# Optimization experiments

Hardware: AMD Instinct MI355X
Metric: run time of the kernel (lower is better)

The kernel has to match this reference:

```python
import jax, jax.numpy as jnp
from jax import lax
import numpy as np

B, T, H, NC = 1024, 2048, 64, 10


def setup_inputs() -> dict:
    key = jax.random.key(0)
    ks = jax.random.split(key, 10)
    s_ih = 1.0 / np.sqrt(H)
    inp = {
        "x": jax.random.normal(ks[0], (B, 1, T), dtype=jnp.float32),
        # PyTorch LSTM params: W_ih [4H, input_size=1], W_hh [4H, H], biases [4H]
        "W_ih": jax.random.uniform(ks[1], (4 * H, 1), minval=-s_ih, maxval=s_ih, dtype=jnp.float32),
        "W_hh": jax.random.uniform(ks[2], (4 * H, H), minval=-s_ih, maxval=s_ih, dtype=jnp.float32),
        "b_ih": jax.random.uniform(ks[3], (4 * H,), minval=-s_ih, maxval=s_ih, dtype=jnp.float32),
        "b_hh": jax.random.uniform(ks[4], (4 * H,), minval=-s_ih, maxval=s_ih, dtype=jnp.float32),
        "fc1_w": jax.random.uniform(ks[5], (H, H), minval=-s_ih, maxval=s_ih, dtype=jnp.float32),
        "fc1_b": jax.random.uniform(ks[6], (H,), minval=-s_ih, maxval=s_ih, dtype=jnp.float32),
        "fc2_w": jax.random.uniform(ks[7], (NC, H), minval=-s_ih, maxval=s_ih, dtype=jnp.float32),
        "fc2_b": jax.random.uniform(ks[8], (NC,), minval=-s_ih, maxval=s_ih, dtype=jnp.float32),
    }
    return inp


def _lstm_last_h(x, W_ih, W_hh, b_ih, b_hh):
    # x: [B, 1, T] -> [B, T, 1]
    xs = jnp.swapaxes(x, 1, 2)
    # precompute input projection for all timesteps: [B, T, 4H]
    x_proj = jnp.einsum("bti,gi->btg", xs, W_ih) + b_ih + b_hh
    x_proj = jnp.swapaxes(x_proj, 0, 1)  # [T, B, 4H]
    h0 = jnp.zeros((x.shape[0], H), dtype=x.dtype)
    c0 = jnp.zeros((x.shape[0], H), dtype=x.dtype)

    def step(carry, xp):
        h, c = carry
        g = xp + h @ W_hh.T  # [B, 4H]
        i, f, gg, o = jnp.split(g, 4, axis=-1)  # PyTorch gate order: i, f, g, o
        i = jax.nn.sigmoid(i)
        f = jax.nn.sigmoid(f)
        gg = jnp.tanh(gg)
        o = jax.nn.sigmoid(o)
        c = f * c + i * gg
        h = o * jnp.tanh(c)
        return (h, c), None

    (h_last, _), _ = lax.scan(step, (h0, c0), x_proj)
    return h_last  # [B, H]


def reference(x, W_ih, W_hh, b_ih, b_hh, fc1_w, fc1_b, fc2_w, fc2_b):
    h = _lstm_last_h(x, W_ih, W_hh, b_ih, b_hh)
    h = jax.nn.relu(h @ fc1_w.T + fc1_b)
    return h @ fc2_w.T + fc2_b  # [B, n_classes]
```

## Files before the change

kernel.cpp:

```cpp
#include <hip/hip_runtime.h>
#include <type_traits>


#define T_STEPS 2048
#define HID 64
#define NCLS 10
#define XCH 128
#define ROWS 4

#define KQS 40
#define KTS 168

typedef short bf16x8 __attribute__((ext_vector_type(8)));
typedef float f32x4 __attribute__((ext_vector_type(4)));

__device__ __forceinline__ unsigned short f2bf(float f) {
    unsigned u = __builtin_bit_cast(unsigned, f);
    u = u + 0x7FFFu + ((u >> 16) & 1u);
    return (unsigned short)(u >> 16);
}

__global__ __attribute__((amdgpu_flat_work_group_size(256, 256)))
void lstm_mfma_kernel(
    const float* __restrict__ x,
    const float* __restrict__ W_ih,
    const float* __restrict__ W_hh,
    const float* __restrict__ b_ih,
    const float* __restrict__ b_hh,
    const float* __restrict__ fc1_w,
    const float* __restrict__ fc1_b,
    const float* __restrict__ fc2_w,
    const float* __restrict__ fc2_b,
    float* __restrict__ out)
{
    const int tid  = threadIdx.x;
    const int lane = tid & 63;
    const int w    = tid >> 6;
    const int quad = lane >> 4;
    const int col  = lane & 15;
    const int row0 = blockIdx.x * ROWS;

    const float L2E = 1.4426950408889634f;

    __shared__ __align__(16) char smem[32768];
    short* whi = (short*)smem;
    short (*abuf)[2 * KTS]     = (short(*)[2 * KTS])smem;
    float (*xlds)[XCH + 4]     = (float(*)[XCH + 4])(smem + 1344);
    float (*hf)[HID + 1]       = (float(*)[HID + 1])(smem + 3456);
    float (*r1buf)[HID + 1]    = (float(*)[HID + 1])(smem + 4496);

    for (int idx = tid; idx < 256 * 64; idx += 256) {
        int r_ = idx >> 6;
        int k  = idx & 63;
        int g = r_ >> 6, u = r_ & 63;
        float scg = (g == 2) ? -2.0f * L2E : -L2E;
        float f = W_hh[r_ * 64 + k] * scg;
        int u4 = u >> 4, n = u & 15;
        int kt = k >> 5, kq = (k & 31) >> 3, j = k & 7;
        int off = (((g * 4 + u4) * 2 + kt) * 64 + (kq * 16 + n)) * 8 + j;
        whi[off] = (short)f2bf(f);
    }
    __syncthreads();

    const int u0 = w * 16 + col;
    bf16x8 Bq[4][2];
    f32x4 biasC[4];
    f32x4 zerov = {0.f, 0.f, 0.f, 0.f};
    #pragma unroll
    for (int gg = 0; gg < 4; ++gg) {
        int t_ = gg * 4 + w;
        #pragma unroll
        for (int kt = 0; kt < 2; ++kt) {
            int off = ((t_ * 2 + kt) * 64 + lane) * 8;
            Bq[gg][kt] = *(const bf16x8*)&whi[off];
            asm volatile("" : "+v"(Bq[gg][kt]));
        }
        float scg = (gg == 2) ? -2.0f * L2E : -L2E;
        float bs = (b_ih[gg * HID + u0] + b_hh[gg * HID + u0]) * scg;
        #pragma unroll
        for (int r = 0; r < 4; ++r) biasC[gg][r] = bs;
    }
    __syncthreads();

    for (int idx = tid; idx < 2 * 2 * KTS; idx += 256) ((short*)abuf)[idx] = 0;

    float wih_u[4];
    #pragma unroll
    for (int gg = 0; gg < 4; ++gg) {
        float scg = (gg == 2) ? -2.0f * L2E : -L2E;
        wih_u[gg] = W_ih[gg * HID + u0] * scg;
    }
    float cc = 0.f, hl = 0.f;

    const int ard0 = (lane >> 4) * KQS + ((lane >> 2) & 3) * 8;
    const int awr  = (u0 >> 5) * KTS + ((u0 >> 3) & 3) * KQS + quad * 8 + (u0 & 7);

    const float* xbase = x + (size_t)row0 * T_STEPS;
    __syncthreads();

    auto step = [&](auto cur_c, int tl) __attribute__((always_inline)) {
        constexpr int CUR = decltype(cur_c)::value;
        constexpr int NXT = CUR ^ 1;

        bf16x8 A0 = *(const bf16x8*)&abuf[CUR][ard0];
        bf16x8 A1 = *(const bf16x8*)&abuf[CUR][ard0 + KTS];

        f32x4 alo[4], ahi[4];
        #pragma unroll
        for (int gg = 0; gg < 4; ++gg)
            alo[gg] = __builtin_amdgcn_mfma_f32_16x16x32_bf16(A0, Bq[gg][0], biasC[gg], 0, 0, 0);
        #pragma unroll
        for (int gg = 0; gg < 4; ++gg)
            ahi[gg] = __builtin_amdgcn_mfma_f32_16x16x32_bf16(A1, Bq[gg][1], zerov, 0, 0, 0);

        {
            float xv = xlds[quad][tl];
            float a0 = fmaf(xv, wih_u[0], alo[0][0] + ahi[0][0]);
            float a1 = fmaf(xv, wih_u[1], alo[1][0] + ahi[1][0]);
            float a2 = fmaf(xv, wih_u[2], alo[2][0] + ahi[2][0]);
            float a3 = fmaf(xv, wih_u[3], alo[3][0] + ahi[3][0]);
            float ig = __builtin_amdgcn_rcpf(1.0f + __builtin_amdgcn_exp2f(a0));
            float fg = __builtin_amdgcn_rcpf(1.0f + __builtin_amdgcn_exp2f(a1));
            float gv = fmaf(2.0f, __builtin_amdgcn_rcpf(1.0f + __builtin_amdgcn_exp2f(a2)), -1.0f);
            float og = __builtin_amdgcn_rcpf(1.0f + __builtin_amdgcn_exp2f(a3));
            cc = fmaf(fg, cc, ig * gv);
            float ec = __builtin_amdgcn_exp2f(-2.8853900817779268f * cc);
            float th = fmaf(2.0f, __builtin_amdgcn_rcpf(1.0f + ec), -1.0f);
            hl = og * th;
            unsigned hp;
            asm("v_cvt_pk_bf16_f32 %0, %1, %2" : "=v"(hp) : "v"(hl), "v"(hl));
            abuf[NXT][awr] = (short)hp;
        }
        __syncthreads();
    };

    #pragma unroll 1
    for (int tc = 0; tc < T_STEPS; tc += 2) {
        const int tl = tc & (XCH - 1);
        if (tl == 0) {
            {
                int i = lane;
                const float* src = xbase + (size_t)w * T_STEPS + tc;
                xlds[w][i]      = src[i];
                xlds[w][i + 64] = src[i + 64];
            }
            __syncthreads();
        }
        step(std::integral_constant<int, 0>{}, tl);
        step(std::integral_constant<int, 1>{}, tl + 1);
    }

    hf[quad][u0] = hl;
    __syncthreads();

    if (w < ROWS) {
        float s = fc1_b[lane];
        const float4* wrow = (const float4*)(fc1_w + lane * HID);
        #pragma unroll
        for (int j4 = 0; j4 < HID / 4; ++j4) {
            float4 wv = wrow[j4];
            s = fmaf(hf[w][j4 * 4 + 0], wv.x, s);
            s = fmaf(hf[w][j4 * 4 + 1], wv.y, s);
            s = fmaf(hf[w][j4 * 4 + 2], wv.z, s);
            s = fmaf(hf[w][j4 * 4 + 3], wv.w, s);
        }
        r1buf[w][lane] = fmaxf(s, 0.0f);
    }
    __syncthreads();

    if (tid < ROWS * NCLS) {
        int m = tid / NCLS, cls = tid % NCLS;
        float s = fc2_b[cls];
        const float* w2 = fc2_w + cls * HID;
        #pragma unroll
        for (int j = 0; j < HID; ++j) s = fmaf(r1buf[m][j], w2[j], s);
        out[(size_t)(row0 + m) * NCLS + cls] = s;
    }
}

extern "C" void kernel_launch(void* const* d_in, const int* in_sizes, int n_in,
                              void* d_out, int out_size, void* d_ws, size_t ws_size,
                              hipStream_t stream) {
    const float* x     = (const float*)d_in[0];
    const float* W_ih  = (const float*)d_in[1];
    const float* W_hh  = (const float*)d_in[2];
    const float* b_ih  = (const float*)d_in[3];
    const float* b_hh  = (const float*)d_in[4];
    const float* fc1_w = (const float*)d_in[5];
    const float* fc1_b = (const float*)d_in[6];
    const float* fc2_w = (const float*)d_in[7];
    const float* fc2_b = (const float*)d_in[8];
    float* out = (float*)d_out;

    dim3 grid(256);
    dim3 block(256);
    lstm_mfma_kernel<<<grid, block, 0, stream>>>(x, W_ih, W_hh, b_ih, b_hh,
                                                 fc1_w, fc1_b, fc2_w, fc2_b, out);
}
```

Baseline: 543.8 us.

## Process two independent batch groups per block and halve the grid

Each block now handles eight batch rows as two interleaved 4-row groups with separate hidden-state buffers, sharing the per-step barrier and the register-resident W_hh fragments. The grid drops from 256 to 128 blocks. The aim is to amortize barrier and latency costs across two independent recurrences through instruction-level parallelism. The cost is that half the compute units sit idle and each step does twice the MFMA and transcendental work.

New measurement: 859.4 us. 1.58x slower.

```diff
diff --git a/kernel.cpp b/kernel.cpp
--- a/kernel.cpp
+++ b/kernel.cpp
@@ -6,7 +6,7 @@
 #define HID 64
 #define NCLS 10
 #define XCH 128
-#define ROWS 4
+#define ROWS 8
 
 #define KQS 40
 #define KTS 168
@@ -44,10 +44,11 @@
 
     __shared__ __align__(16) char smem[32768];
     short* whi = (short*)smem;
-    short (*abuf)[2 * KTS]     = (short(*)[2 * KTS])smem;
-    float (*xlds)[XCH + 4]     = (float(*)[XCH + 4])(smem + 1344);
-    float (*hf)[HID + 1]       = (float(*)[HID + 1])(smem + 3456);
-    float (*r1buf)[HID + 1]    = (float(*)[HID + 1])(smem + 4496);
+    short (*abufA)[2 * KTS]    = (short(*)[2 * KTS])smem;
+    short (*abufB)[2 * KTS]    = (short(*)[2 * KTS])(smem + 1344);
+    float (*xlds)[XCH + 4]     = (float(*)[XCH + 4])(smem + 2688);
+    float (*hf)[HID + 1]       = (float(*)[HID + 1])(smem + 6912);
+    float (*r1buf)[HID + 1]    = (float(*)[HID + 1])(smem + 8992);
 
     for (int idx = tid; idx < 256 * 64; idx += 256) {
         int r_ = idx >> 6;
@@ -82,7 +83,7 @@
     }
     __syncthreads();
 
-    for (int idx = tid; idx < 2 * 2 * KTS; idx += 256) ((short*)abuf)[idx] = 0;
+    for (int idx = tid; idx < 2 * 2 * 2 * KTS; idx += 256) ((short*)smem)[idx] = 0;
 
     float wih_u[4];
     #pragma unroll
@@ -90,7 +91,8 @@
         float scg = (gg == 2) ? -2.0f * L2E : -L2E;
         wih_u[gg] = W_ih[gg * HID + u0] * scg;
     }
-    float cc = 0.f, hl = 0.f;
+    float ccA = 0.f, hlA = 0.f;
+    float ccB = 0.f, hlB = 0.f;
 
     const int ard0 = (lane >> 4) * KQS + ((lane >> 2) & 3) * 8;
     const int awr  = (u0 >> 5) * KTS + ((u0 >> 3) & 3) * KQS + quad * 8 + (u0 & 7);
@@ -102,34 +104,60 @@
         constexpr int CUR = decltype(cur_c)::value;
         constexpr int NXT = CUR ^ 1;
 
-        bf16x8 A0 = *(const bf16x8*)&abuf[CUR][ard0];
-        bf16x8 A1 = *(const bf16x8*)&abuf[CUR][ard0 + KTS];
-
-        f32x4 alo[4], ahi[4];
-        #pragma unroll
-        for (int gg = 0; gg < 4; ++gg)
-            alo[gg] = __builtin_amdgcn_mfma_f32_16x16x32_bf16(A0, Bq[gg][0], biasC[gg], 0, 0, 0);
-        #pragma unroll
-        for (int gg = 0; gg < 4; ++gg)
-            ahi[gg] = __builtin_amdgcn_mfma_f32_16x16x32_bf16(A1, Bq[gg][1], zerov, 0, 0, 0);
+        bf16x8 A0a = *(const bf16x8*)&abufA[CUR][ard0];
+        bf16x8 A1a = *(const bf16x8*)&abufA[CUR][ard0 + KTS];
+        bf16x8 A0b = *(const bf16x8*)&abufB[CUR][ard0];
+        bf16x8 A1b = *(const bf16x8*)&abufB[CUR][ard0 + KTS];
+        float xvA = xlds[quad][tl];
+        float xvB = xlds[quad + 4][tl];
+
+        f32x4 aloA[4], ahiA[4], aloB[4], ahiB[4];
+        #pragma unroll
+        for (int gg = 0; gg < 4; ++gg)
+            aloA[gg] = __builtin_amdgcn_mfma_f32_16x16x32_bf16(A0a, Bq[gg][0], biasC[gg], 0, 0, 0);
+        #pragma unroll
+        for (int gg = 0; gg < 4; ++gg)
+            ahiA[gg] = __builtin_amdgcn_mfma_f32_16x16x32_bf16(A1a, Bq[gg][1], zerov, 0, 0, 0);
+        #pragma unroll
+        for (int gg = 0; gg < 4; ++gg)
+            aloB[gg] = __builtin_amdgcn_mfma_f32_16x16x32_bf16(A0b, Bq[gg][0], biasC[gg], 0, 0, 0);
+        #pragma unroll
+        for (int gg = 0; gg < 4; ++gg)
+            ahiB[gg] = __builtin_amdgcn_mfma_f32_16x16x32_bf16(A1b, Bq[gg][1], zerov, 0, 0, 0);
 
         {
-            float xv = xlds[quad][tl];
-            float a0 = fmaf(xv, wih_u[0], alo[0][0] + ahi[0][0]);
-            float a1 = fmaf(xv, wih_u[1], alo[1][0] + ahi[1][0]);
-            float a2 = fmaf(xv, wih_u[2], alo[2][0] + ahi[2][0]);
-            float a3 = fmaf(xv, wih_u[3], alo[3][0] + ahi[3][0]);
+            float a0 = fmaf(xvA, wih_u[0], aloA[0][0] + ahiA[0][0]);
+            float a1 = fmaf(xvA, wih_u[1], aloA[1][0] + ahiA[1][0]);
+            float a2 = fmaf(xvA, wih_u[2], aloA[2][0] + ahiA[2][0]);
+            float a3 = fmaf(xvA, wih_u[3], aloA[3][0] + ahiA[3][0]);
             float ig = __builtin_amdgcn_rcpf(1.0f + __builtin_amdgcn_exp2f(a0));
             float fg = __builtin_amdgcn_rcpf(1.0f + __builtin_amdgcn_exp2f(a1));
             float gv = fmaf(2.0f, __builtin_amdgcn_rcpf(1.0f + __builtin_amdgcn_exp2f(a2)), -1.0f);
             float og = __builtin_amdgcn_rcpf(1.0f + __builtin_amdgcn_exp2f(a3));
-            cc = fmaf(fg, cc, ig * gv);
-            float ec = __builtin_amdgcn_exp2f(-2.8853900817779268f * cc);
+            ccA = fmaf(fg, ccA, ig * gv);
+            float ec = __builtin_amdgcn_exp2f(-2.8853900817779268f * ccA);
             float th = fmaf(2.0f, __builtin_amdgcn_rcpf(1.0f + ec), -1.0f);
-            hl = og * th;
+            hlA = og * th;
             unsigned hp;
-            asm("v_cvt_pk_bf16_f32 %0, %1, %2" : "=v"(hp) : "v"(hl), "v"(hl));
-            abuf[NXT][awr] = (short)hp;
+            asm("v_cvt_pk_bf16_f32 %0, %1, %2" : "=v"(hp) : "v"(hlA), "v"(hlA));
+            abufA[NXT][awr] = (short)hp;
+        }
+        {
+            float a0 = fmaf(xvB, wih_u[0], aloB[0][0] + ahiB[0][0]);
+            float a1 = fmaf(xvB, wih_u[1], aloB[1][0] + ahiB[1][0]);
+            float a2 = fmaf(xvB, wih_u[2], aloB[2][0] + ahiB[2][0]);
+            float a3 = fmaf(xvB, wih_u[3], aloB[3][0] + ahiB[3][0]);
+            float ig = __builtin_amdgcn_rcpf(1.0f + __builtin_amdgcn_exp2f(a0));
+            float fg = __builtin_amdgcn_rcpf(1.0f + __builtin_amdgcn_exp2f(a1));
+            float gv = fmaf(2.0f, __builtin_amdgcn_rcpf(1.0f + __builtin_amdgcn_exp2f(a2)), -1.0f);
+            float og = __builtin_amdgcn_rcpf(1.0f + __builtin_amdgcn_exp2f(a3));
+            ccB = fmaf(fg, ccB, ig * gv);
+            float ec = __builtin_amdgcn_exp2f(-2.8853900817779268f * ccB);
+            float th = fmaf(2.0f, __builtin_amdgcn_rcpf(1.0f + ec), -1.0f);
+            hlB = og * th;
+            unsigned hp;
+            asm("v_cvt_pk_bf16_f32 %0, %1, %2" : "=v"(hp) : "v"(hlB), "v"(hlB));
+            abufB[NXT][awr] = (short)hp;
         }
         __syncthreads();
     };
@@ -140,9 +168,12 @@
         if (tl == 0) {
             {
                 int i = lane;
-                const float* src = xbase + (size_t)w * T_STEPS + tc;
-                xlds[w][i]      = src[i];
-                xlds[w][i + 64] = src[i + 64];
+                const float* srcA = xbase + (size_t)w * T_STEPS + tc;
+                const float* srcB = xbase + (size_t)(w + 4) * T_STEPS + tc;
+                xlds[w][i]          = srcA[i];
+                xlds[w][i + 64]     = srcA[i + 64];
+                xlds[w + 4][i]      = srcB[i];
+                xlds[w + 4][i + 64] = srcB[i + 64];
             }
             __syncthreads();
         }
@@ -150,21 +181,26 @@
         step(std::integral_constant<int, 1>{}, tl + 1);
     }
 
-    hf[quad][u0] = hl;
-    __syncthreads();
-
-    if (w < ROWS) {
-        float s = fc1_b[lane];
-        const float4* wrow = (const float4*)(fc1_w + lane * HID);
-        #pragma unroll
-        for (int j4 = 0; j4 < HID / 4; ++j4) {
-            float4 wv = wrow[j4];
-            s = fmaf(hf[w][j4 * 4 + 0], wv.x, s);
-            s = fmaf(hf[w][j4 * 4 + 1], wv.y, s);
-            s = fmaf(hf[w][j4 * 4 + 2], wv.z, s);
-            s = fmaf(hf[w][j4 * 4 + 3], wv.w, s);
-        }
-        r1buf[w][lane] = fmaxf(s, 0.0f);
+    hf[quad][u0]     = hlA;
+    hf[quad + 4][u0] = hlB;
+    __syncthreads();
+
+    {
+        #pragma unroll
+        for (int grp = 0; grp < 2; ++grp) {
+            int m = w + grp * 4;
+            float s = fc1_b[lane];
+            const float4* wrow = (const float4*)(fc1_w + lane * HID);
+            #pragma unroll
+            for (int j4 = 0; j4 < HID / 4; ++j4) {
+                float4 wv = wrow[j4];
+                s = fmaf(hf[m][j4 * 4 + 0], wv.x, s);
+                s = fmaf(hf[m][j4 * 4 + 1], wv.y, s);
+                s = fmaf(hf[m][j4 * 4 + 2], wv.z, s);
+                s = fmaf(hf[m][j4 * 4 + 3], wv.w, s);
+            }
+            r1buf[m][lane] = fmaxf(s, 0.0f);
+        }
     }
     __syncthreads();
 
@@ -192,7 +228,7 @@
     const float* fc2_b = (const float*)d_in[8];
     float* out = (float*)d_out;
 
-    dim3 grid(256);
+    dim3 grid(128);
     dim3 block(256);
     lstm_mfma_kernel<<<grid, block, 0, stream>>>(x, W_ih, W_hh, b_ih, b_hh,
                                                  fc1_w, fc1_b, fc2_w, fc2_b, out);
```
